# Optimization experiments

Hardware: AMD Instinct MI355X
Metric: run time of the kernel (lower is better)

Reference implementation:

```python
import jax, jax.numpy as jnp
import numpy as np

N = 50000
E = 800000
D_IN = 128
D_OUT = 128
LN_EPS = 1e-5
DROP_P = 0.1


def setup_inputs() -> dict:
    key = jax.random.key(0)
    ks = jax.random.split(key, 8)
    x = jax.random.normal(ks[0], (N, D_IN), dtype=jnp.float32)
    edge_index = jax.random.randint(ks[1], (2, E), 0, N, dtype=jnp.int64)
    # dropout mask: binary keep-mask scaled by 1/(1-p), as torch dropout produces
    u = jax.random.uniform(ks[2], (N, D_IN), dtype=jnp.float32)
    dropout_mask = (u > DROP_P).astype(jnp.float32) / (1.0 - DROP_P)
    # LayerNorm affine params
    gamma = jnp.ones((D_IN,), dtype=jnp.float32)
    beta = jnp.zeros((D_IN,), dtype=jnp.float32)
    # SAGEConv linears: lin_l (aggregated neighbors, with bias), lin_r (root, no bias)
    s = 1.0 / np.sqrt(D_IN)
    w_l = jax.random.uniform(ks[3], (D_OUT, D_IN), minval=-s, maxval=s, dtype=jnp.float32)
    b_l = jax.random.uniform(ks[4], (D_OUT,), minval=-s, maxval=s, dtype=jnp.float32)
    w_r = jax.random.uniform(ks[5], (D_OUT, D_IN), minval=-s, maxval=s, dtype=jnp.float32)
    return {"x": x, "edge_index": edge_index, "dropout_mask": dropout_mask,
            "gamma": gamma, "beta": beta, "w_l": w_l, "b_l": b_l, "w_r": w_r}


def reference(x, edge_index, dropout_mask, gamma, beta, w_l, b_l, w_r):
    # LayerNorm + ReLU + dropout mask
    mu = jnp.mean(x, axis=-1, keepdims=True)
    var = jnp.mean(jnp.square(x - mu), axis=-1, keepdims=True)
    h = (x - mu) * jax.lax.rsqrt(var + LN_EPS) * gamma + beta
    h = jax.nn.relu(h) * dropout_mask  # [N, D_IN]
    # SAGEConv: mean-aggregate source features into target nodes
    src = edge_index[0]
    dst = edge_index[1]
    msg = h[src]  # [E, D_IN] gathered messages
    agg = jax.ops.segment_sum(msg, dst, num_segments=N)  # [N, D_IN]
    deg = jax.ops.segment_sum(jnp.ones((E,), dtype=h.dtype), dst, num_segments=N)
    agg = agg / jnp.maximum(deg, 1.0)[:, None]
    # out = lin_l(agg) + lin_r(h)
    out = agg @ w_l.T + b_l + h @ w_r.T  # [N, D_OUT]
    return out
```

## Files before the change

### kernel.cpp

```cpp
#include <hip/hip_runtime.h>
#include <hip/hip_bf16.h>

#define N_NODES 50000
#define N_EDGES 800000
#define D 128
#define NB_SCAN ((N_NODES + 255) / 256)

typedef short bf16x8 __attribute__((ext_vector_type(8)));
typedef float f32x4 __attribute__((ext_vector_type(4)));

__device__ __forceinline__ unsigned int bf16u(float f) {
  __hip_bfloat16 b = __float2bfloat16(f);
  return (unsigned int)*reinterpret_cast<unsigned short*>(&b);
}

__global__ __launch_bounds__(256) void ln_kernel(
    const float* __restrict__ x, const float* __restrict__ mask,
    const float* __restrict__ gamma, const float* __restrict__ beta,
    unsigned int* __restrict__ hb) {
  const int l = threadIdx.x & 63;
  const int n = blockIdx.x * 4 + (threadIdx.x >> 6);
  const float2 xv = ((const float2*)x)[(size_t)n * 64 + l];
  float s = xv.x + xv.y;
  float q = xv.x * xv.x + xv.y * xv.y;
#pragma unroll
  for (int m = 1; m < 64; m <<= 1) {
    s += __shfl_xor(s, m);
    q += __shfl_xor(q, m);
  }
  const float mean = s * (1.0f / 128.0f);
  const float var = q * (1.0f / 128.0f) - mean * mean;
  const float rs = rsqrtf(var + 1e-5f);
  const float2 gv = ((const float2*)gamma)[l];
  const float2 bv = ((const float2*)beta)[l];
  const float2 mv = ((const float2*)mask)[(size_t)n * 64 + l];
  const float h0 = fmaxf((xv.x - mean) * rs * gv.x + bv.x, 0.0f) * mv.x;
  const float h1 = fmaxf((xv.y - mean) * rs * gv.y + bv.y, 0.0f) * mv.y;
  hb[(size_t)n * 64 + l] = (bf16u(h1) << 16) | bf16u(h0);
}

__global__ __launch_bounds__(256) void wt_kernel(
    const float* __restrict__ w_l, const float* __restrict__ w_r,
    unsigned int* __restrict__ wtb) {
  const int i = blockIdx.x * 256 + threadIdx.x;
  const float* src = (i < 8192) ? w_l : w_r;
  const int j = (i < 8192) ? 2 * i : 2 * (i - 8192);
  wtb[i] = (bf16u(src[j + 1]) << 16) | bf16u(src[j]);
}

__global__ __launch_bounds__(256) void gemm_kernel(
    const unsigned short* __restrict__ hb, const unsigned short* __restrict__ wtb,
    const float* __restrict__ b_l, unsigned int* __restrict__ gb,
    float* __restrict__ r) {
  __shared__ float lds[64][65];
  const int t = threadIdx.x;
  const int w = t >> 6;
  const int l = t & 63;
  const int lm = l & 15;
  const int quad = l >> 4;
  const int nb = blockIdx.x * 64;
  const int by = blockIdx.y;

  int anode = nb + w * 16 + lm;
  if (anode >= N_NODES) anode = N_NODES - 1;
  const unsigned short* arow = hb + (size_t)anode * D + quad * 8;
  bf16x8 af[4];
#pragma unroll
  for (int ch = 0; ch < 4; ++ch)
    af[ch] = *(const bf16x8*)(arow + ch * 32);

  const unsigned short* brow = wtb + (size_t)(by * 64 + lm) * D + quad * 8;
  bf16x8 bf[4][4];
#pragma unroll
  for (int sub = 0; sub < 4; ++sub)
#pragma unroll
    for (int ch = 0; ch < 4; ++ch)
      bf[sub][ch] = *(const bf16x8*)(brow + sub * 16 * D + ch * 32);

  f32x4 acc[4];
#pragma unroll
  for (int sub = 0; sub < 4; ++sub) acc[sub] = (f32x4){0.f, 0.f, 0.f, 0.f};
#pragma unroll
  for (int ch = 0; ch < 4; ++ch)
#pragma unroll
    for (int sub = 0; sub < 4; ++sub)
      acc[sub] = __builtin_amdgcn_mfma_f32_16x16x32_bf16(af[ch], bf[sub][ch],
                                                         acc[sub], 0, 0, 0);

#pragma unroll
  for (int sub = 0; sub < 4; ++sub)
#pragma unroll
    for (int reg = 0; reg < 4; ++reg)
      lds[w * 16 + quad * 4 + reg][sub * 16 + lm] = acc[sub][reg];
  __syncthreads();

  if (by < 2) {
#pragma unroll
    for (int i = 0; i < 2; ++i) {
      const int row = (t >> 3) + i * 32;
      const int grp = t & 7;
      const int node = nb + row;
      if (node < N_NODES) {
        const float* lr = &lds[row][grp * 8];
        uint4 p;
        p.x = (bf16u(lr[1]) << 16) | bf16u(lr[0]);
        p.y = (bf16u(lr[3]) << 16) | bf16u(lr[2]);
        p.z = (bf16u(lr[5]) << 16) | bf16u(lr[4]);
        p.w = (bf16u(lr[7]) << 16) | bf16u(lr[6]);
        ((uint4*)gb)[(size_t)node * 16 + by * 8 + grp] = p;
      }
    }
  } else {
    const int row = t >> 2;
    const int grp = t & 3;
    const int node = nb + row;
    const int col0 = (by - 2) * 64 + grp * 16;
    if (node < N_NODES) {
#pragma unroll
      for (int qd = 0; qd < 4; ++qd) {
        const float4 bv = *(const float4*)(b_l + col0 + qd * 4);
        const float* lr = &lds[row][grp * 16 + qd * 4];
        float4 o;
        o.x = lr[0] + bv.x;
        o.y = lr[1] + bv.y;
        o.z = lr[2] + bv.z;
        o.w = lr[3] + bv.w;
        *(float4*)(r + (size_t)node * D + col0 + qd * 4) = o;
      }
    }
  }
}

__global__ __launch_bounds__(256) void hist_kernel(const int* __restrict__ ei,
                                                   int* __restrict__ deg,
                                                   int* __restrict__ rank) {
  const int e = blockIdx.x * 256 + threadIdx.x;
  if (e < N_EDGES) rank[e] = atomicAdd(&deg[ei[N_EDGES + e]], 1);
}

__global__ __launch_bounds__(256) void scan1_kernel(
    const int* __restrict__ deg, int* __restrict__ offsets,
    int* __restrict__ partial) {
  __shared__ int sm[256];
  const int t = threadIdx.x;
  const int i = blockIdx.x * 256 + t;
  const int v = (i < N_NODES) ? deg[i] : 0;
  sm[t] = v;
  __syncthreads();
#pragma unroll
  for (int ofs = 1; ofs < 256; ofs <<= 1) {
    int x = sm[t];
    if (t >= ofs) x += sm[t - ofs];
    __syncthreads();
    sm[t] = x;
    __syncthreads();
  }
  if (i < N_NODES) offsets[i] = sm[t] - v;
  if (t == 255) partial[blockIdx.x] = sm[255];
}

__global__ __launch_bounds__(256) void scan2_kernel(int* __restrict__ partial) {
  __shared__ int sm[256];
  const int t = threadIdx.x;
  const int v = (t < NB_SCAN) ? partial[t] : 0;
  sm[t] = v;
  __syncthreads();
#pragma unroll
  for (int ofs = 1; ofs < 256; ofs <<= 1) {
    int x = sm[t];
    if (t >= ofs) x += sm[t - ofs];
    __syncthreads();
    sm[t] = x;
    __syncthreads();
  }
  if (t < NB_SCAN) partial[t] = sm[t] - v;
}

__global__ __launch_bounds__(256) void scan3_kernel(
    int* __restrict__ offsets, const int* __restrict__ partial) {
  const int i = blockIdx.x * 256 + threadIdx.x;
  if (i < N_NODES) offsets[i] += partial[blockIdx.x];
  if (i == 0) offsets[N_NODES] = N_EDGES;
}

__global__ __launch_bounds__(256) void scatter_kernel(
    const int* __restrict__ ei, const int* __restrict__ offsets,
    const int* __restrict__ rank, int* __restrict__ csr) {
  const int e = blockIdx.x * 256 + threadIdx.x;
  if (e < N_EDGES) {
    const int dst = ei[N_EDGES + e];
    csr[offsets[dst] + rank[e]] = ei[e];
  }
}

#define ACC8(v)                                     \
  do {                                              \
    acc[0] += __uint_as_float((v).x << 16);         \
    acc[1] += __uint_as_float((v).x & 0xffff0000u); \
    acc[2] += __uint_as_float((v).y << 16);         \
    acc[3] += __uint_as_float((v).y & 0xffff0000u); \
    acc[4] += __uint_as_float((v).z << 16);         \
    acc[5] += __uint_as_float((v).z & 0xffff0000u); \
    acc[6] += __uint_as_float((v).w << 16);         \
    acc[7] += __uint_as_float((v).w & 0xffff0000u); \
  } while (0)

__global__ __launch_bounds__(256) void agg_kernel(
    const int* __restrict__ offsets, const int* __restrict__ csr,
    const unsigned int* __restrict__ gb, const float* __restrict__ r,
    float* __restrict__ out) {
  const int l = threadIdx.x & 63;
  const int q = l >> 4;
  const int c = l & 15;
  const int n = blockIdx.x * 4 + (threadIdx.x >> 6);
  const int s = offsets[n];
  const int e = offsets[n + 1];
  const uint4* g4 = (const uint4*)gb;
  float acc[8];
#pragma unroll
  for (int k = 0; k < 8; ++k) acc[k] = 0.0f;
  for (int base = s; base < e; base += 64) {
    const int cnt = min(e - base, 64);
    int idx = (l < cnt) ? csr[base + l] : 0;
    int j = 0;
    for (; j + 16 <= cnt; j += 16) {
      const int i0 = __shfl(idx, j + 0 + q);
      const int i1 = __shfl(idx, j + 4 + q);
      const int i2 = __shfl(idx, j + 8 + q);
      const int i3 = __shfl(idx, j + 12 + q);
      const uint4 v0 = g4[(size_t)i0 * 16 + c];
      const uint4 v1 = g4[(size_t)i1 * 16 + c];
      const uint4 v2 = g4[(size_t)i2 * 16 + c];
      const uint4 v3 = g4[(size_t)i3 * 16 + c];
      ACC8(v0);
      ACC8(v1);
      ACC8(v2);
      ACC8(v3);
    }
    for (; j + 4 <= cnt; j += 4) {
      const int i0 = __shfl(idx, j + q);
      const uint4 v0 = g4[(size_t)i0 * 16 + c];
      ACC8(v0);
    }
    if (j < cnt) {
      const int rem = cnt - j;
      const int i0 = __shfl(idx, j + min(q, rem - 1));
      if (q < rem) {
        const uint4 v0 = g4[(size_t)i0 * 16 + c];
        ACC8(v0);
      }
    }
  }
#pragma unroll
  for (int k = 0; k < 8; ++k) {
    acc[k] += __shfl_xor(acc[k], 16);
    acc[k] += __shfl_xor(acc[k], 32);
  }
  if (l < 16) {
    const float inv = 1.0f / fmaxf((float)(e - s), 1.0f);
    const float4 r0 = ((const float4*)r)[(size_t)n * 32 + c * 2 + 0];
    const float4 r1 = ((const float4*)r)[(size_t)n * 32 + c * 2 + 1];
    float4 o0, o1;
    o0.x = fmaf(acc[0], inv, r0.x);
    o0.y = fmaf(acc[1], inv, r0.y);
    o0.z = fmaf(acc[2], inv, r0.z);
    o0.w = fmaf(acc[3], inv, r0.w);
    o1.x = fmaf(acc[4], inv, r1.x);
    o1.y = fmaf(acc[5], inv, r1.y);
    o1.z = fmaf(acc[6], inv, r1.z);
    o1.w = fmaf(acc[7], inv, r1.w);
    ((float4*)out)[(size_t)n * 32 + c * 2 + 0] = o0;
    ((float4*)out)[(size_t)n * 32 + c * 2 + 1] = o1;
  }
}

extern "C" void kernel_launch(void* const* d_in, const int* in_sizes, int n_in,
                              void* d_out, int out_size, void* d_ws,
                              size_t ws_size, hipStream_t stream) {
  const float* x = (const float*)d_in[0];
  const int* ei = (const int*)d_in[1];
  const float* mask = (const float*)d_in[2];
  const float* gamma = (const float*)d_in[3];
  const float* beta = (const float*)d_in[4];
  const float* w_l = (const float*)d_in[5];
  const float* b_l = (const float*)d_in[6];
  const float* w_r = (const float*)d_in[7];
  float* out = (float*)d_out;

  char* ws = (char*)d_ws;
  size_t off = 0;
  auto alloc = [&](size_t bytes) {
    char* p = ws + off;
    off += (bytes + 255) & ~(size_t)255;
    return p;
  };
  unsigned int* hb =
      (unsigned int*)alloc((size_t)N_NODES * D * sizeof(unsigned short));
  unsigned int* gb =
      (unsigned int*)alloc((size_t)N_NODES * D * sizeof(unsigned short));
  float* r = (float*)alloc((size_t)N_NODES * D * sizeof(float));
  unsigned int* wtb =
      (unsigned int*)alloc((size_t)2 * D * D * sizeof(unsigned short));
  int* deg = (int*)alloc((size_t)N_NODES * sizeof(int));
  int* offsets = (int*)alloc((size_t)(N_NODES + 1) * sizeof(int));
  int* partial = (int*)alloc((size_t)NB_SCAN * sizeof(int));
  int* rank = (int*)alloc((size_t)N_EDGES * sizeof(int));
  int* csr = (int*)alloc((size_t)N_EDGES * sizeof(int));

  hipMemsetAsync(deg, 0, (size_t)N_NODES * sizeof(int), stream);
  wt_kernel<<<64, 256, 0, stream>>>(w_l, w_r, wtb);
  ln_kernel<<<N_NODES / 4, 256, 0, stream>>>(x, mask, gamma, beta, hb);
  gemm_kernel<<<dim3((N_NODES + 63) / 64, 4), 256, 0, stream>>>(
      (const unsigned short*)hb, (const unsigned short*)wtb, b_l, gb, r);
  hist_kernel<<<N_EDGES / 256, 256, 0, stream>>>(ei, deg, rank);
  scan1_kernel<<<NB_SCAN, 256, 0, stream>>>(deg, offsets, partial);
  scan2_kernel<<<1, 256, 0, stream>>>(partial);
  scan3_kernel<<<NB_SCAN, 256, 0, stream>>>(offsets, partial);
  scatter_kernel<<<N_EDGES / 256, 256, 0, stream>>>(ei, offsets, rank, csr);
  agg_kernel<<<N_NODES / 4, 256, 0, stream>>>(offsets, csr, gb, r, out);
}
```

Measured before the change: 240.3 us.

## Fuse GEMM column tiles, drop scan3 pass, vectorise hist/scatter edges

The GEMM now computes all 256 output columns per 64-node block. Weights are staged in LDS and results are written straight from MFMA accumulators in a permuted column order, with no LDS transpose. The scan3 kernel is removed: consumers add the block partial to the local offset on the fly. Hist and scatter each process four edges per thread with int4 loads, and agg undoes the column permutation with strided scalar stores. This cuts launches, redundant A-tile reads and LDS round-trips, at the cost of more accumulator registers, higher LDS use and less coalesced output stores.

```diff
diff --git a/kernel.cpp b/kernel.cpp
--- a/kernel.cpp
+++ b/kernel.cpp
@@ -49,84 +49,72 @@
 }
 
 __global__ __launch_bounds__(256) void gemm_kernel(
-    const unsigned short* __restrict__ hb, const unsigned short* __restrict__ wtb,
-    const float* __restrict__ b_l, unsigned int* __restrict__ gb,
-    float* __restrict__ r) {
-  __shared__ float lds[64][65];
+    const unsigned short* __restrict__ hb,
+    const unsigned short* __restrict__ wtb, const float* __restrict__ b_l,
+    unsigned int* __restrict__ gb, float* __restrict__ rp) {
+  __shared__ unsigned short Bs[64 * 64 * 8];
   const int t = threadIdx.x;
   const int w = t >> 6;
   const int l = t & 63;
   const int lm = l & 15;
   const int quad = l >> 4;
   const int nb = blockIdx.x * 64;
-  const int by = blockIdx.y;
 
   int anode = nb + w * 16 + lm;
   if (anode >= N_NODES) anode = N_NODES - 1;
   const unsigned short* arow = hb + (size_t)anode * D + quad * 8;
   bf16x8 af[4];
 #pragma unroll
-  for (int ch = 0; ch < 4; ++ch)
-    af[ch] = *(const bf16x8*)(arow + ch * 32);
-
-  const unsigned short* brow = wtb + (size_t)(by * 64 + lm) * D + quad * 8;
-  bf16x8 bf[4][4];
-#pragma unroll
-  for (int sub = 0; sub < 4; ++sub)
+  for (int ch = 0; ch < 4; ++ch) af[ch] = *(const bf16x8*)(arow + ch * 32);
+
+#pragma unroll
+  for (int i = 0; i < 16; ++i) {
+    const int fid = w * 16 + i;
+    const int sub = fid >> 2;
+    const int ch = fid & 3;
+    const uint4 v = *(const uint4*)(wtb + (size_t)(sub * 16 + lm) * D +
+                                    ch * 32 + quad * 8);
+    *(uint4*)(Bs + ((size_t)fid * 64 + l) * 8) = v;
+  }
+  __syncthreads();
+
+  f32x4 acc[16];
+#pragma unroll
+  for (int sub = 0; sub < 16; ++sub) acc[sub] = (f32x4){0.f, 0.f, 0.f, 0.f};
+  const bf16x8* BsF = (const bf16x8*)Bs;
+#pragma unroll
+  for (int sub = 0; sub < 16; ++sub)
 #pragma unroll
     for (int ch = 0; ch < 4; ++ch)
-      bf[sub][ch] = *(const bf16x8*)(brow + sub * 16 * D + ch * 32);
-
-  f32x4 acc[4];
-#pragma unroll
-  for (int sub = 0; sub < 4; ++sub) acc[sub] = (f32x4){0.f, 0.f, 0.f, 0.f};
-#pragma unroll
-  for (int ch = 0; ch < 4; ++ch)
-#pragma unroll
-    for (int sub = 0; sub < 4; ++sub)
-      acc[sub] = __builtin_amdgcn_mfma_f32_16x16x32_bf16(af[ch], bf[sub][ch],
-                                                         acc[sub], 0, 0, 0);
-
-#pragma unroll
-  for (int sub = 0; sub < 4; ++sub)
-#pragma unroll
-    for (int reg = 0; reg < 4; ++reg)
-      lds[w * 16 + quad * 4 + reg][sub * 16 + lm] = acc[sub][reg];
-  __syncthreads();
-
-  if (by < 2) {
-#pragma unroll
-    for (int i = 0; i < 2; ++i) {
-      const int row = (t >> 3) + i * 32;
-      const int grp = t & 7;
-      const int node = nb + row;
-      if (node < N_NODES) {
-        const float* lr = &lds[row][grp * 8];
-        uint4 p;
-        p.x = (bf16u(lr[1]) << 16) | bf16u(lr[0]);
-        p.y = (bf16u(lr[3]) << 16) | bf16u(lr[2]);
-        p.z = (bf16u(lr[5]) << 16) | bf16u(lr[4]);
-        p.w = (bf16u(lr[7]) << 16) | bf16u(lr[6]);
-        ((uint4*)gb)[(size_t)node * 16 + by * 8 + grp] = p;
-      }
-    }
-  } else {
-    const int row = t >> 2;
-    const int grp = t & 3;
-    const int node = nb + row;
-    const int col0 = (by - 2) * 64 + grp * 16;
+      acc[sub] = __builtin_amdgcn_mfma_f32_16x16x32_bf16(
+          af[ch], BsF[(sub * 4 + ch) * 64 + l], acc[sub], 0, 0, 0);
+
+  float blv[8];
+#pragma unroll
+  for (int j = 0; j < 8; ++j) blv[j] = b_l[j * 16 + lm];
+
+  const int node0 = nb + w * 16 + quad * 4;
+#pragma unroll
+  for (int reg = 0; reg < 4; ++reg) {
+    const int node = node0 + reg;
     if (node < N_NODES) {
-#pragma unroll
-      for (int qd = 0; qd < 4; ++qd) {
-        const float4 bv = *(const float4*)(b_l + col0 + qd * 4);
-        const float* lr = &lds[row][grp * 16 + qd * 4];
-        float4 o;
-        o.x = lr[0] + bv.x;
-        o.y = lr[1] + bv.y;
-        o.z = lr[2] + bv.z;
-        o.w = lr[3] + bv.w;
-        *(float4*)(r + (size_t)node * D + col0 + qd * 4) = o;
-      }
+      uint4 p;
+      p.x = (bf16u(acc[1][reg]) << 16) | bf16u(acc[0][reg]);
+      p.y = (bf16u(acc[3][reg]) << 16) | bf16u(acc[2][reg]);
+      p.z = (bf16u(acc[5][reg]) << 16) | bf16u(acc[4][reg]);
+      p.w = (bf16u(acc[7][reg]) << 16) | bf16u(acc[6][reg]);
+      ((uint4*)gb)[(size_t)node * 16 + lm] = p;
+      float4 q0, q1;
+      q0.x = acc[8][reg] + blv[0];
+      q0.y = acc[9][reg] + blv[1];
+      q0.z = acc[10][reg] + blv[2];
+      q0.w = acc[11][reg] + blv[3];
+      q1.x = acc[12][reg] + blv[4];
+      q1.y = acc[13][reg] + blv[5];
+      q1.z = acc[14][reg] + blv[6];
+      q1.w = acc[15][reg] + blv[7];
+      ((float4*)rp)[(size_t)node * 32 + lm * 2 + 0] = q0;
+      ((float4*)rp)[(size_t)node * 32 + lm * 2 + 1] = q1;
     }
   }
 }
@@ -134,12 +122,23 @@
 __global__ __launch_bounds__(256) void hist_kernel(const int* __restrict__ ei,
                                                    int* __restrict__ deg,
                                                    int* __restrict__ rank) {
-  const int e = blockIdx.x * 256 + threadIdx.x;
-  if (e < N_EDGES) rank[e] = atomicAdd(&deg[ei[N_EDGES + e]], 1);
+  const int e = (blockIdx.x * 256 + threadIdx.x) * 4;
+  if (e + 3 < N_EDGES) {
+    const int4 d4 = *(const int4*)(ei + N_EDGES + e);
+    int4 r4;
+    r4.x = atomicAdd(&deg[d4.x], 1);
+    r4.y = atomicAdd(&deg[d4.y], 1);
+    r4.z = atomicAdd(&deg[d4.z], 1);
+    r4.w = atomicAdd(&deg[d4.w], 1);
+    *(int4*)(rank + e) = r4;
+  } else {
+    for (int k = e; k < N_EDGES; ++k)
+      rank[k] = atomicAdd(&deg[ei[N_EDGES + k]], 1);
+  }
 }
 
 __global__ __launch_bounds__(256) void scan1_kernel(
-    const int* __restrict__ deg, int* __restrict__ offsets,
+    const int* __restrict__ deg, int* __restrict__ offL1,
     int* __restrict__ partial) {
   __shared__ int sm[256];
   const int t = threadIdx.x;
@@ -155,7 +154,7 @@
     sm[t] = x;
     __syncthreads();
   }
-  if (i < N_NODES) offsets[i] = sm[t] - v;
+  if (i < N_NODES) offL1[i] = sm[t] - v;
   if (t == 255) partial[blockIdx.x] = sm[255];
 }
 
@@ -176,20 +175,24 @@
   if (t < NB_SCAN) partial[t] = sm[t] - v;
 }
 
-__global__ __launch_bounds__(256) void scan3_kernel(
-    int* __restrict__ offsets, const int* __restrict__ partial) {
-  const int i = blockIdx.x * 256 + threadIdx.x;
-  if (i < N_NODES) offsets[i] += partial[blockIdx.x];
-  if (i == 0) offsets[N_NODES] = N_EDGES;
-}
-
 __global__ __launch_bounds__(256) void scatter_kernel(
-    const int* __restrict__ ei, const int* __restrict__ offsets,
-    const int* __restrict__ rank, int* __restrict__ csr) {
-  const int e = blockIdx.x * 256 + threadIdx.x;
-  if (e < N_EDGES) {
-    const int dst = ei[N_EDGES + e];
-    csr[offsets[dst] + rank[e]] = ei[e];
+    const int* __restrict__ ei, const int* __restrict__ offL1,
+    const int* __restrict__ partial, const int* __restrict__ rank,
+    int* __restrict__ csr) {
+  const int e = (blockIdx.x * 256 + threadIdx.x) * 4;
+  if (e + 3 < N_EDGES) {
+    const int4 s4 = *(const int4*)(ei + e);
+    const int4 d4 = *(const int4*)(ei + N_EDGES + e);
+    const int4 r4 = *(const int4*)(rank + e);
+    csr[offL1[d4.x] + partial[d4.x >> 8] + r4.x] = s4.x;
+    csr[offL1[d4.y] + partial[d4.y >> 8] + r4.y] = s4.y;
+    csr[offL1[d4.z] + partial[d4.z >> 8] + r4.z] = s4.z;
+    csr[offL1[d4.w] + partial[d4.w >> 8] + r4.w] = s4.w;
+  } else {
+    for (int k = e; k < N_EDGES; ++k) {
+      const int dst = ei[N_EDGES + k];
+      csr[offL1[dst] + partial[dst >> 8] + rank[k]] = ei[k];
+    }
   }
 }
 
@@ -206,15 +209,16 @@
   } while (0)
 
 __global__ __launch_bounds__(256) void agg_kernel(
-    const int* __restrict__ offsets, const int* __restrict__ csr,
-    const unsigned int* __restrict__ gb, const float* __restrict__ r,
-    float* __restrict__ out) {
+    const int* __restrict__ offL1, const int* __restrict__ partial,
+    const int* __restrict__ csr, const unsigned int* __restrict__ gb,
+    const float* __restrict__ rp, float* __restrict__ out) {
   const int l = threadIdx.x & 63;
   const int q = l >> 4;
   const int c = l & 15;
   const int n = blockIdx.x * 4 + (threadIdx.x >> 6);
-  const int s = offsets[n];
-  const int e = offsets[n + 1];
+  const int s = offL1[n] + partial[n >> 8];
+  const int e = (n + 1 < N_NODES) ? offL1[n + 1] + partial[(n + 1) >> 8]
+                                  : N_EDGES;
   const uint4* g4 = (const uint4*)gb;
   float acc[8];
 #pragma unroll
@@ -258,19 +262,17 @@
   }
   if (l < 16) {
     const float inv = 1.0f / fmaxf((float)(e - s), 1.0f);
-    const float4 r0 = ((const float4*)r)[(size_t)n * 32 + c * 2 + 0];
-    const float4 r1 = ((const float4*)r)[(size_t)n * 32 + c * 2 + 1];
-    float4 o0, o1;
-    o0.x = fmaf(acc[0], inv, r0.x);
-    o0.y = fmaf(acc[1], inv, r0.y);
-    o0.z = fmaf(acc[2], inv, r0.z);
-    o0.w = fmaf(acc[3], inv, r0.w);
-    o1.x = fmaf(acc[4], inv, r1.x);
-    o1.y = fmaf(acc[5], inv, r1.y);
-    o1.z = fmaf(acc[6], inv, r1.z);
-    o1.w = fmaf(acc[7], inv, r1.w);
-    ((float4*)out)[(size_t)n * 32 + c * 2 + 0] = o0;
-    ((float4*)out)[(size_t)n * 32 + c * 2 + 1] = o1;
+    const float4 rp0 = ((const float4*)rp)[(size_t)n * 32 + c * 2 + 0];
+    const float4 rp1 = ((const float4*)rp)[(size_t)n * 32 + c * 2 + 1];
+    float* o = out + (size_t)n * D + c;
+    o[0]   = fmaf(acc[0], inv, rp0.x);
+    o[16]  = fmaf(acc[1], inv, rp0.y);
+    o[32]  = fmaf(acc[2], inv, rp0.z);
+    o[48]  = fmaf(acc[3], inv, rp0.w);
+    o[64]  = fmaf(acc[4], inv, rp1.x);
+    o[80]  = fmaf(acc[5], inv, rp1.y);
+    o[96]  = fmaf(acc[6], inv, rp1.z);
+    o[112] = fmaf(acc[7], inv, rp1.w);
   }
 }
 
@@ -298,11 +300,11 @@
       (unsigned int*)alloc((size_t)N_NODES * D * sizeof(unsigned short));
   unsigned int* gb =
       (unsigned int*)alloc((size_t)N_NODES * D * sizeof(unsigned short));
-  float* r = (float*)alloc((size_t)N_NODES * D * sizeof(float));
+  float* rp = (float*)alloc((size_t)N_NODES * D * sizeof(float));
   unsigned int* wtb =
       (unsigned int*)alloc((size_t)2 * D * D * sizeof(unsigned short));
   int* deg = (int*)alloc((size_t)N_NODES * sizeof(int));
-  int* offsets = (int*)alloc((size_t)(N_NODES + 1) * sizeof(int));
+  int* offL1 = (int*)alloc((size_t)N_NODES * sizeof(int));
   int* partial = (int*)alloc((size_t)NB_SCAN * sizeof(int));
   int* rank = (int*)alloc((size_t)N_EDGES * sizeof(int));
   int* csr = (int*)alloc((size_t)N_EDGES * sizeof(int));
@@ -310,12 +312,13 @@
   hipMemsetAsync(deg, 0, (size_t)N_NODES * sizeof(int), stream);
   wt_kernel<<<64, 256, 0, stream>>>(w_l, w_r, wtb);
   ln_kernel<<<N_NODES / 4, 256, 0, stream>>>(x, mask, gamma, beta, hb);
-  gemm_kernel<<<dim3((N_NODES + 63) / 64, 4), 256, 0, stream>>>(
-      (const unsigned short*)hb, (const unsigned short*)wtb, b_l, gb, r);
-  hist_kernel<<<N_EDGES / 256, 256, 0, stream>>>(ei, deg, rank);
-  scan1_kernel<<<NB_SCAN, 256, 0, stream>>>(deg, offsets, partial);
+  gemm_kernel<<<(N_NODES + 63) / 64, 256, 0, stream>>>(
+      (const unsigned short*)hb, (const unsigned short*)wtb, b_l, gb, rp);
+  hist_kernel<<<(N_EDGES / 4 + 255) / 256, 256, 0, stream>>>(ei, deg, rank);
+  scan1_kernel<<<NB_SCAN, 256, 0, stream>>>(deg, offL1, partial);
   scan2_kernel<<<1, 256, 0, stream>>>(partial);
-  scan3_kernel<<<NB_SCAN, 256, 0, stream>>>(offsets, partial);
-  scatter_kernel<<<N_EDGES / 256, 256, 0, stream>>>(ei, offsets, rank, csr);
-  agg_kernel<<<N_NODES / 4, 256, 0, stream>>>(offsets, csr, gb, r, out);
-}
+  scatter_kernel<<<(N_EDGES / 4 + 255) / 256, 256, 0, stream>>>(
+      ei, offL1, partial, rank, csr);
+  agg_kernel<<<N_NODES / 4, 256, 0, stream>>>(offL1, partial, csr, gb, rp,
+                                              out);
+}
```

New measurement: 218.9 us. -8.9%, faster.
